# Optimization experiments

Hardware: AMD Instinct MI355X
Metric: run time of the kernel (lower is better)

## Reference

```python
import jax, jax.numpy as jnp
import numpy as np

DIM = 256
HEADS = 8
P = 8   # patch_size
S = 4   # stride


def _pos_index(p):
    # Swin-style relative position index, computed statically in numpy
    coord = np.arange(p)
    ii, jj = np.meshgrid(coord, coord, indexing='ij')
    cf = np.stack([ii.ravel(), jj.ravel()])              # [2, p*p]
    rel = cf[:, :, None] - cf[:, None, :]                # [2, P, P]
    rel = rel.transpose(1, 2, 0).copy()                  # [P, P, 2]
    rel[:, :, 0] += p - 1
    rel[:, :, 1] += p - 1
    rel[:, :, 0] *= 2 * p - 1
    return jnp.asarray(rel.sum(-1))                      # [P, P] int


def setup_inputs() -> dict:
    key = jax.random.key(0)
    k1, k2, k3, k4, k5 = jax.random.split(key, 5)
    x = jax.random.normal(k1, (2, DIM, 96, 96), jnp.float32)
    # depthwise 1x1 conv on 3*dim channels -> per-channel scale + bias
    qkv_w = jax.random.normal(k2, (3 * DIM,), jnp.float32) * 0.1 + 1.0
    qkv_b = jax.random.normal(k3, (3 * DIM,), jnp.float32) * 0.1
    # 1x1 conv dim->dim, no bias
    out_w = jax.random.normal(k4, (DIM, DIM), jnp.float32) * 0.05
    # relative position bias table, trunc_normal(std=0.02)
    pos_table = jax.random.normal(k5, ((2 * P - 1) ** 2, HEADS), jnp.float32) * 0.02
    return {"x": x, "qkv_w": qkv_w, "qkv_b": qkv_b, "out_w": out_w, "pos_table": pos_table}


def reference(x, qkv_w, qkv_b, out_w, pos_table):
    B, C, H, W = x.shape
    h, p, s = HEADS, P, S
    d = C // h
    pad = p - s
    # replicate pad right/bottom
    xp = jnp.pad(x, ((0, 0), (0, 0), (0, pad), (0, pad)), mode='edge')
    x3 = jnp.concatenate([xp, xp, xp], axis=1)           # [B, 3C, Hp, Wp]
    # depthwise 1x1 conv == per-channel affine
    qkv = x3 * qkv_w[None, :, None, None] + qkv_b[None, :, None, None]
    n = (H + pad - p) // s + 1                           # patches per side
    idx = (jnp.arange(n) * s)[:, None] + jnp.arange(p)[None, :]   # [n, p]
    # unfold: extract overlapping p x p patches with stride s
    t = qkv[:, :, idx, :]                                # [B, 3C, n, p, Wp]
    t = t[:, :, :, :, idx]                               # [B, 3C, n, p, n, p]
    t = t.transpose(0, 1, 2, 4, 3, 5)                    # [B, 3C, n, n, p, p]
    t = t.reshape(B, 3, h, d, n * n, p * p).transpose(1, 0, 2, 4, 5, 3)  # [3,B,h,N,P,d]
    q, k, v = t[0] * (d ** -0.5), t[1], t[2]
    bias = pos_table[_pos_index(p)]                      # [P, P, h]
    bias = bias.transpose(2, 0, 1)                       # [h, P, P]
    attn = jnp.einsum('bhnqd,bhnkd->bhnqk', q, k) + bias[None, :, None]
    attn = jax.nn.softmax(attn, axis=-1)
    out = jnp.einsum('bhnqk,bhnkd->bhnqd', attn, v)      # [B, h, N, P, d]
    # keep only the top-left stride x stride of each patch, then fold (non-overlap)
    out = out.reshape(B, h, n, n, p, p, d)[:, :, :, :, :s, :s]   # [B,h,n,n,s,s,d]
    out = out.transpose(0, 1, 6, 2, 4, 3, 5).reshape(B, C, H, W)
    return jnp.einsum('oc,bchw->bohw', out_w, out)
```

## Files before the change

### kernel.cpp

```cpp
#include <hip/hip_runtime.h>

typedef float f4 __attribute__((ext_vector_type(4)));
typedef float f32x4 __attribute__((ext_vector_type(4)));
typedef __bf16 bf16x8 __attribute__((ext_vector_type(8)));
typedef __bf16 bf16x4 __attribute__((ext_vector_type(4)));

#define NPSIDE 24

#define XS(ch_, r_, c_) xs[(ch_) * 169 + (r_) * 21 + (c_)]

__global__ __launch_bounds__(256, 4) void patch_attn(
    const float* __restrict__ x,
    const float* __restrict__ qkv_w,
    const float* __restrict__ qkv_b,
    const float* __restrict__ pos_table,
    const float* __restrict__ wmat,
    __bf16* __restrict__ mid,
    __bf16* __restrict__ wbf)
{
    __shared__ float xs[32 * 169];
    __shared__ __bf16 Ps[4][16][72];

    const int t = threadIdx.x;

    if (blockIdx.x < 64) {
        const int i = (blockIdx.x * 256 + t) * 4;
        const int o = i >> 8, c = i & 255;
        const f4 v = *(const f4*)&wmat[i];
        bf16x4 ov;
        #pragma unroll
        for (int j = 0; j < 4; ++j) ov[j] = (__bf16)v[j];
        *(bf16x4*)&wbf[((o >> 4) * 8 + (c >> 5)) * 512 + (o & 15) * 32 + (c & 31)] = ov;
    }

    const int raw = blockIdx.x;
    const int sw  = (raw & 7) * 288 + (raw >> 3);
    const int bh  = sw / 144;
    const int r   = sw % 144;
    const int head = bh & 7;
    const int b    = bh >> 3;
    const int ni   = r / 6;
    const int nj0p = (r % 6) * 4;
    const int c0   = head * 32;

    #pragma unroll
    for (int i = 0; i < 5; ++i) {
        const int idx = i * 256 + t;
        const int ch  = idx / 40;
        const int rem = idx % 40;
        const int row = rem / 5, cg = rem % 5;
        const int rg  = min(4 * ni + row, 95);
        const int cg4 = 16 * (r % 6) + 4 * cg;
        const float* xrow = x + (((size_t)b * 256 + c0 + ch) * 96 + rg) * 96;
        f4 v;
        if (cg4 <= 92) {
            v = *(const f4*)&xrow[cg4];
        } else {
            const float s = xrow[95];
            v = (f4){s, s, s, s};
        }
        float* xdst = &XS(ch, row, 4 * cg);
        xdst[0] = v.x; xdst[1] = v.y; xdst[2] = v.z; xdst[3] = v.w;
    }

    const int wv = t >> 6, l = t & 63;
    const int l16 = l & 15, lg = l >> 4;
    const float qscale = 0.17677669529663687f;

    float kw8[8], kb8[8], qw8[8], qb8[8];
    #pragma unroll
    for (int j = 0; j < 8; ++j) {
        const int c = c0 + 8 * lg + j;
        kw8[j] = qkv_w[256 + c];
        kb8[j] = qkv_b[256 + c];
        qw8[j] = qkv_w[c] * qscale;
        qb8[j] = qkv_b[c] * qscale;
    }
    float vw2[2], vb2[2];
    #pragma unroll
    for (int nt = 0; nt < 2; ++nt) {
        const int c = c0 + nt * 16 + l16;
        vw2[nt] = qkv_w[512 + c];
        vb2[nt] = qkv_b[512 + c];
    }

    __syncthreads();

    const int nj  = nj0p + wv;
    const int cbl = 4 * wv;

    bf16x8 qf;
    {
        const int qrow = l16 >> 2, qcol = cbl + (l16 & 3);
        #pragma unroll
        for (int j = 0; j < 8; ++j)
            qf[j] = (__bf16)(XS(8 * lg + j, qrow, qcol) * qw8[j] + qb8[j]);
    }

    const f32x4 zf = {0.f, 0.f, 0.f, 0.f};
    f32x4 sacc[4];
    #pragma unroll
    for (int t4 = 0; t4 < 4; ++t4) {
        const int px = l16 + 16 * t4;
        const int kr = px >> 3, kc = cbl + (px & 7);
        bf16x8 kf;
        #pragma unroll
        for (int j = 0; j < 8; ++j)
            kf[j] = (__bf16)(XS(8 * lg + j, kr, kc) * kw8[j] + kb8[j]);
        sacc[t4] = __builtin_amdgcn_mfma_f32_16x16x32_bf16(qf, kf, zf, 0, 0, 0);
    }

    float sv[4][4], rinv[4];
    #pragma unroll
    for (int rr = 0; rr < 4; ++rr) {
        const int qrow = lg * 4 + rr;
        const int qi = qrow >> 2, qj = qrow & 3;
        float m = -1e30f;
        #pragma unroll
        for (int t4 = 0; t4 < 4; ++t4) {
            const int kcol = l16 + 16 * t4;
            const int ki = kcol >> 3, kj = kcol & 7;
            const float s = sacc[t4][rr]
                + pos_table[((qi - ki + 7) * 15 + (qj - kj + 7)) * 8 + head];
            sv[t4][rr] = s;
            m = fmaxf(m, s);
        }
        #pragma unroll
        for (int off = 8; off >= 1; off >>= 1)
            m = fmaxf(m, __shfl_xor(m, off, 16));
        float sum = 0.f;
        #pragma unroll
        for (int t4 = 0; t4 < 4; ++t4) {
            const float p = __expf(sv[t4][rr] - m);
            sv[t4][rr] = p;
            sum += p;
        }
        #pragma unroll
        for (int off = 8; off >= 1; off >>= 1)
            sum += __shfl_xor(sum, off, 16);
        rinv[rr] = 1.0f / sum;
        #pragma unroll
        for (int t4 = 0; t4 < 4; ++t4)
            Ps[wv][qrow][l16 + 16 * t4] = (__bf16)sv[t4][rr];
    }

    f32x4 oa = zf, ob = zf;
    #pragma unroll
    for (int kt = 0; kt < 2; ++kt) {
        bf16x8 pf = *(const bf16x8*)&Ps[wv][l16][lg * 8 + 32 * kt];
        bf16x8 v0, v1;
        #pragma unroll
        for (int j = 0; j < 8; ++j) {
            const int px = kt * 32 + 8 * lg + j;
            const int vr = px >> 3, vc = cbl + (px & 7);
            v0[j] = (__bf16)(XS(l16,      vr, vc) * vw2[0] + vb2[0]);
            v1[j] = (__bf16)(XS(16 + l16, vr, vc) * vw2[1] + vb2[1]);
        }
        oa = __builtin_amdgcn_mfma_f32_16x16x32_bf16(pf, v0, oa, 0, 0, 0);
        ob = __builtin_amdgcn_mfma_f32_16x16x32_bf16(pf, v1, ob, 0, 0, 0);
    }

    const int pbase = ni * 384 + lg * 96 + nj * 4;
    __bf16* mbb = mid + (size_t)b * 9216 * 256;
    #pragma unroll
    for (int rr = 0; rr < 4; ++rr) {
        const int p = pbase + rr;
        __bf16* dst = mbb + ((p >> 4) * 8 + head) * 512 + (p & 15) * 32;
        dst[l16]      = (__bf16)(oa[rr] * rinv[rr]);
        dst[16 + l16] = (__bf16)(ob[rr] * rinv[rr]);
    }
}

__global__ __launch_bounds__(256) void proj(
    const __bf16* __restrict__ wbf,
    const __bf16* __restrict__ mid,
    float* __restrict__ y)
{
    __shared__ __align__(16) __bf16 wlds[4][8][512];

    const int t  = threadIdx.x;
    const int wv = t >> 6;
    const int l  = t & 63;
    const int l16 = l & 15, lg = l >> 4;
    const int fragoff = l16 * 32 + lg * 8;

    const int raw = blockIdx.x;
    const int xcd = raw & 7;
    const int seq = raw >> 3;
    const int chunk = xcd * 18 + (seq >> 3);
    const int rem   = seq & 7;
    const int b     = rem >> 2;
    const int og4   = rem & 3;
    const int ot0   = og4 * 4;
    const int pt    = chunk * 4 + wv;

    {
        const bf16x8* wsrc = (const bf16x8*)&wbf[(size_t)ot0 * 8 * 512];
        bf16x8* wdst = (bf16x8*)&wlds[0][0][0];
        #pragma unroll
        for (int i = 0; i < 8; ++i)
            wdst[t + 256 * i] = wsrc[t + 256 * i];
    }
    __syncthreads();

    const __bf16* midb = mid + ((size_t)b * 9216 + (size_t)pt * 16) * 256;
    bf16x8 bfr[8];
    #pragma unroll
    for (int kt = 0; kt < 8; ++kt)
        bfr[kt] = *(const bf16x8*)&midb[kt * 512 + fragoff];

    f32x4 acc[4];
    #pragma unroll
    for (int ot = 0; ot < 4; ++ot) acc[ot] = (f32x4){0.f, 0.f, 0.f, 0.f};

    #pragma unroll
    for (int ot = 0; ot < 4; ++ot)
        #pragma unroll
        for (int kt = 0; kt < 8; ++kt) {
            const bf16x8 af = *(const bf16x8*)&wlds[ot][kt][fragoff];
            acc[ot] = __builtin_amdgcn_mfma_f32_16x16x32_bf16(af, bfr[kt], acc[ot], 0, 0, 0);
        }

    const int p = pt * 16 + l16;
    #pragma unroll
    for (int ot = 0; ot < 4; ++ot) {
        const int o = (ot0 + ot) * 16 + lg * 4;
        float* yb = y + ((size_t)b * 256 + o) * 9216 + p;
        #pragma unroll
        for (int r = 0; r < 4; ++r)
            yb[(size_t)r * 9216] = acc[ot][r];
    }
}

extern "C" void kernel_launch(void* const* d_in, const int* in_sizes, int n_in,
                              void* d_out, int out_size, void* d_ws, size_t ws_size,
                              hipStream_t stream) {
    const float* x         = (const float*)d_in[0];
    const float* qkv_w     = (const float*)d_in[1];
    const float* qkv_b     = (const float*)d_in[2];
    const float* out_w     = (const float*)d_in[3];
    const float* pos_table = (const float*)d_in[4];
    float* y    = (float*)d_out;
    __bf16* mid = (__bf16*)d_ws;
    __bf16* wbf = (__bf16*)((char*)d_ws + (12u << 20));

    patch_attn<<<dim3(2304), dim3(256), 0, stream>>>(
        x, qkv_w, qkv_b, pos_table, out_w, mid, wbf);
    proj<<<dim3(1152), dim3(256), 0, stream>>>(
        wbf, mid, y);
}
```

Baseline: 34.79 us.

## Fuse patch attention with output projection, one block per patch

Merges the attention kernel and the 1x1 projection kernel into one kernel. Each block now handles one patch across all 8 heads, with each wave doing two heads, and keeps the per-patch attention output in LDS. The block then multiplies it by the bf16 weight, which is read straight from global memory and prepared by a small separate conversion kernel. This removes the bf16 intermediate round-trip through global memory, but the x tile is no longer shared across neighbouring patches, the weight is re-read per block, and the y stores become strided 4-wide writes.

Result: slower. 48.75 us (+40.2%).

```diff
diff --git a/kernel.cpp b/kernel.cpp
--- a/kernel.cpp
+++ b/kernel.cpp
@@ -5,230 +5,186 @@
 typedef __bf16 bf16x8 __attribute__((ext_vector_type(8)));
 typedef __bf16 bf16x4 __attribute__((ext_vector_type(4)));
 
-#define NPSIDE 24
-
-#define XS(ch_, r_, c_) xs[(ch_) * 169 + (r_) * 21 + (c_)]
-
-__global__ __launch_bounds__(256, 4) void patch_attn(
+__global__ __launch_bounds__(256) void wcvt(
+    const float* __restrict__ wmat, __bf16* __restrict__ wbf)
+{
+    const int i = (blockIdx.x * 256 + threadIdx.x) * 4;
+    const int o = i >> 8, c = i & 255;
+    const f4 v = *(const f4*)&wmat[i];
+    bf16x4 ov;
+    #pragma unroll
+    for (int j = 0; j < 4; ++j) ov[j] = (__bf16)v[j];
+    *(bf16x4*)&wbf[((o >> 4) * 8 + (c >> 5)) * 512 + (o & 15) * 32 + (c & 31)] = ov;
+}
+
+#define XSW(ch_, r_, c_) xsw[wv][(ch_) * 65 + (r_) * 8 + (c_)]
+
+__global__ __launch_bounds__(256) void fused_attn_proj(
     const float* __restrict__ x,
     const float* __restrict__ qkv_w,
     const float* __restrict__ qkv_b,
     const float* __restrict__ pos_table,
-    const float* __restrict__ wmat,
-    __bf16* __restrict__ mid,
-    __bf16* __restrict__ wbf)
+    const __bf16* __restrict__ wbf,
+    float* __restrict__ y)
 {
-    __shared__ float xs[32 * 169];
+    __shared__ float  xsw[4][32 * 65];
+    __shared__ __bf16 midt[8][16][40];
     __shared__ __bf16 Ps[4][16][72];
 
     const int t = threadIdx.x;
-
-    if (blockIdx.x < 64) {
-        const int i = (blockIdx.x * 256 + t) * 4;
-        const int o = i >> 8, c = i & 255;
-        const f4 v = *(const f4*)&wmat[i];
-        bf16x4 ov;
-        #pragma unroll
-        for (int j = 0; j < 4; ++j) ov[j] = (__bf16)v[j];
-        *(bf16x4*)&wbf[((o >> 4) * 8 + (c >> 5)) * 512 + (o & 15) * 32 + (c & 31)] = ov;
-    }
-
-    const int raw = blockIdx.x;
-    const int sw  = (raw & 7) * 288 + (raw >> 3);
-    const int bh  = sw / 144;
-    const int r   = sw % 144;
-    const int head = bh & 7;
-    const int b    = bh >> 3;
-    const int ni   = r / 6;
-    const int nj0p = (r % 6) * 4;
-    const int c0   = head * 32;
-
-    #pragma unroll
-    for (int i = 0; i < 5; ++i) {
-        const int idx = i * 256 + t;
-        const int ch  = idx / 40;
-        const int rem = idx % 40;
-        const int row = rem / 5, cg = rem % 5;
-        const int rg  = min(4 * ni + row, 95);
-        const int cg4 = 16 * (r % 6) + 4 * cg;
-        const float* xrow = x + (((size_t)b * 256 + c0 + ch) * 96 + rg) * 96;
-        f4 v;
-        if (cg4 <= 92) {
-            v = *(const f4*)&xrow[cg4];
-        } else {
-            const float s = xrow[95];
-            v = (f4){s, s, s, s};
-        }
-        float* xdst = &XS(ch, row, 4 * cg);
-        xdst[0] = v.x; xdst[1] = v.y; xdst[2] = v.z; xdst[3] = v.w;
-    }
-
     const int wv = t >> 6, l = t & 63;
     const int l16 = l & 15, lg = l >> 4;
+
+    const int raw = blockIdx.x;
+    const int sw = (raw & 7) * 144 + (raw >> 3);
+    const int b = sw / 576;
+    const int patch = sw % 576;
+    const int ni = patch / 24, nj = patch % 24;
     const float qscale = 0.17677669529663687f;
-
-    float kw8[8], kb8[8], qw8[8], qb8[8];
-    #pragma unroll
-    for (int j = 0; j < 8; ++j) {
-        const int c = c0 + 8 * lg + j;
-        kw8[j] = qkv_w[256 + c];
-        kb8[j] = qkv_b[256 + c];
-        qw8[j] = qkv_w[c] * qscale;
-        qb8[j] = qkv_b[c] * qscale;
+    const f32x4 zf = {0.f, 0.f, 0.f, 0.f};
+
+    const int ch4 = l >> 4, srow = (l >> 1) & 7, scg = l & 1;
+    const int rg = min(4 * ni + srow, 95);
+
+    #pragma unroll
+    for (int hp = 0; hp < 2; ++hp) {
+        const int h = 2 * wv + hp;
+        const int c0 = h * 32;
+
+        #pragma unroll
+        for (int d = 0; d < 8; ++d) {
+            const int ch = ch4 * 8 + d;
+            const float* xpl = x + (size_t)(b * 256 + c0 + ch) * 9216;
+            f4 v;
+            if (nj == 23 && scg == 1) {
+                const float s = xpl[rg * 96 + 95];
+                v = (f4){s, s, s, s};
+            } else {
+                v = *(const f4*)&xpl[rg * 96 + 4 * nj + 4 * scg];
+            }
+            float* dst = &XSW(ch, srow, 4 * scg);
+            dst[0] = v.x; dst[1] = v.y; dst[2] = v.z; dst[3] = v.w;
+        }
+
+        float kw8[8], kb8[8], qw8[8], qb8[8];
+        #pragma unroll
+        for (int j = 0; j < 8; ++j) {
+            const int c = c0 + 8 * lg + j;
+            kw8[j] = qkv_w[256 + c];
+            kb8[j] = qkv_b[256 + c];
+            qw8[j] = qkv_w[c] * qscale;
+            qb8[j] = qkv_b[c] * qscale;
+        }
+        float vw2[2], vb2[2];
+        #pragma unroll
+        for (int nt = 0; nt < 2; ++nt) {
+            const int c = c0 + nt * 16 + l16;
+            vw2[nt] = qkv_w[512 + c];
+            vb2[nt] = qkv_b[512 + c];
+        }
+
+        bf16x8 qf;
+        {
+            const int qr = l16 >> 2, qc = l16 & 3;
+            #pragma unroll
+            for (int j = 0; j < 8; ++j)
+                qf[j] = (__bf16)(XSW(8 * lg + j, qr, qc) * qw8[j] + qb8[j]);
+        }
+
+        f32x4 sacc[4];
+        #pragma unroll
+        for (int t4 = 0; t4 < 4; ++t4) {
+            const int px = l16 + 16 * t4;
+            const int kr = px >> 3, kc = px & 7;
+            bf16x8 kf;
+            #pragma unroll
+            for (int j = 0; j < 8; ++j)
+                kf[j] = (__bf16)(XSW(8 * lg + j, kr, kc) * kw8[j] + kb8[j]);
+            sacc[t4] = __builtin_amdgcn_mfma_f32_16x16x32_bf16(qf, kf, zf, 0, 0, 0);
+        }
+
+        float sv[4][4], rinv[4];
+        #pragma unroll
+        for (int rr = 0; rr < 4; ++rr) {
+            const int qrow = lg * 4 + rr;
+            const int qi = qrow >> 2, qj = qrow & 3;
+            float m = -1e30f;
+            #pragma unroll
+            for (int t4 = 0; t4 < 4; ++t4) {
+                const int kcol = l16 + 16 * t4;
+                const int ki = kcol >> 3, kj = kcol & 7;
+                const float s = sacc[t4][rr]
+                    + pos_table[((qi - ki + 7) * 15 + (qj - kj + 7)) * 8 + h];
+                sv[t4][rr] = s;
+                m = fmaxf(m, s);
+            }
+            #pragma unroll
+            for (int off = 8; off >= 1; off >>= 1)
+                m = fmaxf(m, __shfl_xor(m, off, 16));
+            float sum = 0.f;
+            #pragma unroll
+            for (int t4 = 0; t4 < 4; ++t4) {
+                const float p = __expf(sv[t4][rr] - m);
+                sv[t4][rr] = p;
+                sum += p;
+            }
+            #pragma unroll
+            for (int off = 8; off >= 1; off >>= 1)
+                sum += __shfl_xor(sum, off, 16);
+            rinv[rr] = 1.0f / sum;
+            #pragma unroll
+            for (int t4 = 0; t4 < 4; ++t4)
+                Ps[wv][qrow][l16 + 16 * t4] = (__bf16)sv[t4][rr];
+        }
+
+        f32x4 oa = zf, ob = zf;
+        #pragma unroll
+        for (int kt = 0; kt < 2; ++kt) {
+            bf16x8 pf = *(const bf16x8*)&Ps[wv][l16][lg * 8 + 32 * kt];
+            bf16x8 v0, v1;
+            #pragma unroll
+            for (int j = 0; j < 8; ++j) {
+                const int vr = 4 * kt + lg;
+                v0[j] = (__bf16)(XSW(l16,      vr, j) * vw2[0] + vb2[0]);
+                v1[j] = (__bf16)(XSW(16 + l16, vr, j) * vw2[1] + vb2[1]);
+            }
+            oa = __builtin_amdgcn_mfma_f32_16x16x32_bf16(pf, v0, oa, 0, 0, 0);
+            ob = __builtin_amdgcn_mfma_f32_16x16x32_bf16(pf, v1, ob, 0, 0, 0);
+        }
+
+        #pragma unroll
+        for (int rr = 0; rr < 4; ++rr) {
+            const int qrow = lg * 4 + rr;
+            midt[h][qrow][l16]      = (__bf16)(oa[rr] * rinv[rr]);
+            midt[h][qrow][16 + l16] = (__bf16)(ob[rr] * rinv[rr]);
+        }
     }
-    float vw2[2], vb2[2];
-    #pragma unroll
-    for (int nt = 0; nt < 2; ++nt) {
-        const int c = c0 + nt * 16 + l16;
-        vw2[nt] = qkv_w[512 + c];
-        vb2[nt] = qkv_b[512 + c];
-    }
 
     __syncthreads();
 
-    const int nj  = nj0p + wv;
-    const int cbl = 4 * wv;
-
-    bf16x8 qf;
-    {
-        const int qrow = l16 >> 2, qcol = cbl + (l16 & 3);
-        #pragma unroll
-        for (int j = 0; j < 8; ++j)
-            qf[j] = (__bf16)(XS(8 * lg + j, qrow, qcol) * qw8[j] + qb8[j]);
-    }
-
-    const f32x4 zf = {0.f, 0.f, 0.f, 0.f};
-    f32x4 sacc[4];
-    #pragma unroll
-    for (int t4 = 0; t4 < 4; ++t4) {
-        const int px = l16 + 16 * t4;
-        const int kr = px >> 3, kc = cbl + (px & 7);
-        bf16x8 kf;
-        #pragma unroll
-        for (int j = 0; j < 8; ++j)
-            kf[j] = (__bf16)(XS(8 * lg + j, kr, kc) * kw8[j] + kb8[j]);
-        sacc[t4] = __builtin_amdgcn_mfma_f32_16x16x32_bf16(qf, kf, zf, 0, 0, 0);
-    }
-
-    float sv[4][4], rinv[4];
-    #pragma unroll
-    for (int rr = 0; rr < 4; ++rr) {
-        const int qrow = lg * 4 + rr;
-        const int qi = qrow >> 2, qj = qrow & 3;
-        float m = -1e30f;
-        #pragma unroll
-        for (int t4 = 0; t4 < 4; ++t4) {
-            const int kcol = l16 + 16 * t4;
-            const int ki = kcol >> 3, kj = kcol & 7;
-            const float s = sacc[t4][rr]
-                + pos_table[((qi - ki + 7) * 15 + (qj - kj + 7)) * 8 + head];
-            sv[t4][rr] = s;
-            m = fmaxf(m, s);
-        }
-        #pragma unroll
-        for (int off = 8; off >= 1; off >>= 1)
-            m = fmaxf(m, __shfl_xor(m, off, 16));
-        float sum = 0.f;
-        #pragma unroll
-        for (int t4 = 0; t4 < 4; ++t4) {
-            const float p = __expf(sv[t4][rr] - m);
-            sv[t4][rr] = p;
-            sum += p;
-        }
-        #pragma unroll
-        for (int off = 8; off >= 1; off >>= 1)
-            sum += __shfl_xor(sum, off, 16);
-        rinv[rr] = 1.0f / sum;
-        #pragma unroll
-        for (int t4 = 0; t4 < 4; ++t4)
-            Ps[wv][qrow][l16 + 16 * t4] = (__bf16)sv[t4][rr];
-    }
-
-    f32x4 oa = zf, ob = zf;
-    #pragma unroll
-    for (int kt = 0; kt < 2; ++kt) {
-        bf16x8 pf = *(const bf16x8*)&Ps[wv][l16][lg * 8 + 32 * kt];
-        bf16x8 v0, v1;
-        #pragma unroll
-        for (int j = 0; j < 8; ++j) {
-            const int px = kt * 32 + 8 * lg + j;
-            const int vr = px >> 3, vc = cbl + (px & 7);
-            v0[j] = (__bf16)(XS(l16,      vr, vc) * vw2[0] + vb2[0]);
-            v1[j] = (__bf16)(XS(16 + l16, vr, vc) * vw2[1] + vb2[1]);
-        }
-        oa = __builtin_amdgcn_mfma_f32_16x16x32_bf16(pf, v0, oa, 0, 0, 0);
-        ob = __builtin_amdgcn_mfma_f32_16x16x32_bf16(pf, v1, ob, 0, 0, 0);
-    }
-
-    const int pbase = ni * 384 + lg * 96 + nj * 4;
-    __bf16* mbb = mid + (size_t)b * 9216 * 256;
-    #pragma unroll
-    for (int rr = 0; rr < 4; ++rr) {
-        const int p = pbase + rr;
-        __bf16* dst = mbb + ((p >> 4) * 8 + head) * 512 + (p & 15) * 32;
-        dst[l16]      = (__bf16)(oa[rr] * rinv[rr]);
-        dst[16 + l16] = (__bf16)(ob[rr] * rinv[rr]);
-    }
-}
-
-__global__ __launch_bounds__(256) void proj(
-    const __bf16* __restrict__ wbf,
-    const __bf16* __restrict__ mid,
-    float* __restrict__ y)
-{
-    __shared__ __align__(16) __bf16 wlds[4][8][512];
-
-    const int t  = threadIdx.x;
-    const int wv = t >> 6;
-    const int l  = t & 63;
-    const int l16 = l & 15, lg = l >> 4;
+    bf16x8 bfr[8];
+    #pragma unroll
+    for (int kt = 0; kt < 8; ++kt)
+        bfr[kt] = *(const bf16x8*)&midt[kt][l16][lg * 8];
+
     const int fragoff = l16 * 32 + lg * 8;
-
-    const int raw = blockIdx.x;
-    const int xcd = raw & 7;
-    const int seq = raw >> 3;
-    const int chunk = xcd * 18 + (seq >> 3);
-    const int rem   = seq & 7;
-    const int b     = rem >> 2;
-    const int og4   = rem & 3;
-    const int ot0   = og4 * 4;
-    const int pt    = chunk * 4 + wv;
-
-    {
-        const bf16x8* wsrc = (const bf16x8*)&wbf[(size_t)ot0 * 8 * 512];
-        bf16x8* wdst = (bf16x8*)&wlds[0][0][0];
-        #pragma unroll
-        for (int i = 0; i < 8; ++i)
-            wdst[t + 256 * i] = wsrc[t + 256 * i];
-    }
-    __syncthreads();
-
-    const __bf16* midb = mid + ((size_t)b * 9216 + (size_t)pt * 16) * 256;
-    bf16x8 bfr[8];
-    #pragma unroll
-    for (int kt = 0; kt < 8; ++kt)
-        bfr[kt] = *(const bf16x8*)&midb[kt * 512 + fragoff];
-
-    f32x4 acc[4];
-    #pragma unroll
-    for (int ot = 0; ot < 4; ++ot) acc[ot] = (f32x4){0.f, 0.f, 0.f, 0.f};
-
-    #pragma unroll
-    for (int ot = 0; ot < 4; ++ot)
+    const int hh = 4 * ni + (l16 >> 2), ww = 4 * nj + (l16 & 3);
+    const size_t ybase = (size_t)b * 256 * 9216 + hh * 96 + ww;
+
+    #pragma unroll
+    for (int i = 0; i < 4; ++i) {
+        const int ot = 4 * wv + i;
+        f32x4 acc = zf;
         #pragma unroll
         for (int kt = 0; kt < 8; ++kt) {
-            const bf16x8 af = *(const bf16x8*)&wlds[ot][kt][fragoff];
-            acc[ot] = __builtin_amdgcn_mfma_f32_16x16x32_bf16(af, bfr[kt], acc[ot], 0, 0, 0);
-        }
-
-    const int p = pt * 16 + l16;
-    #pragma unroll
-    for (int ot = 0; ot < 4; ++ot) {
-        const int o = (ot0 + ot) * 16 + lg * 4;
-        float* yb = y + ((size_t)b * 256 + o) * 9216 + p;
-        #pragma unroll
-        for (int r = 0; r < 4; ++r)
-            yb[(size_t)r * 9216] = acc[ot][r];
+            const bf16x8 af = *(const bf16x8*)&wbf[(ot * 8 + kt) * 512 + fragoff];
+            acc = __builtin_amdgcn_mfma_f32_16x16x32_bf16(af, bfr[kt], acc, 0, 0, 0);
+        }
+        #pragma unroll
+        for (int rr = 0; rr < 4; ++rr) {
+            const int o = ot * 16 + lg * 4 + rr;
+            y[ybase + (size_t)o * 9216] = acc[rr];
+        }
     }
 }
 
@@ -241,11 +197,9 @@
     const float* out_w     = (const float*)d_in[3];
     const float* pos_table = (const float*)d_in[4];
     float* y    = (float*)d_out;
-    __bf16* mid = (__bf16*)d_ws;
-    __bf16* wbf = (__bf16*)((char*)d_ws + (12u << 20));
-
-    patch_attn<<<dim3(2304), dim3(256), 0, stream>>>(
-        x, qkv_w, qkv_b, pos_table, out_w, mid, wbf);
-    proj<<<dim3(1152), dim3(256), 0, stream>>>(
-        wbf, mid, y);
+    __bf16* wbf = (__bf16*)d_ws;
+
+    wcvt<<<dim3(64), dim3(256), 0, stream>>>(out_w, wbf);
+    fused_attn_proj<<<dim3(1152), dim3(256), 0, stream>>>(
+        x, qkv_w, qkv_b, pos_table, wbf, y);
 }
```
